# Optimization experiments

Measured on AMD Instinct MI355X. Metric: run time of the kernel, lower is better.

The kernel has to match this reference:

```python
import jax, jax.numpy as jnp
import numpy as np

DIM = 1024
N_HEADS = 16
HEAD_DIM = DIM // N_HEADS


def setup_inputs() -> dict:
    key = jax.random.key(0)
    ks = jax.random.split(key, 6)
    s = DIM ** -0.5
    return {
        "x": jax.random.normal(ks[0], (2, 2048, DIM), dtype=jnp.float32),
        "Wq": jax.random.normal(ks[1], (DIM, DIM), dtype=jnp.float32) * s,
        "Wk": jax.random.normal(ks[2], (DIM, DIM), dtype=jnp.float32) * s,
        "Wv": jax.random.normal(ks[3], (DIM, DIM), dtype=jnp.float32) * s,
        "Wo": jax.random.normal(ks[4], (DIM, DIM), dtype=jnp.float32) * s,
        "bo": jax.random.normal(ks[5], (DIM,), dtype=jnp.float32) * 0.01,
    }


def reference(x, Wq, Wk, Wv, Wo, bo):
    B, T, C = x.shape
    H, D = N_HEADS, HEAD_DIM
    # Linear(dim, dim, bias=False): y = x @ W^T
    q = (x @ Wq.T).reshape(B, T, H, D).transpose(0, 2, 1, 3)  # B H T D
    k = (x @ Wk.T).reshape(B, T, H, D).transpose(0, 2, 1, 3)
    v = (x @ Wv.T).reshape(B, T, H, D).transpose(0, 2, 1, 3)
    q = q * (D ** -0.5)
    attn = jnp.einsum('bhqd,bhkd->bhqk', q, k)  # B H T T
    causal_mask = jnp.triu(jnp.ones((T, T), dtype=bool), k=1)
    attn = jnp.where(causal_mask, -jnp.inf, attn)
    attn = jax.nn.softmax(attn, axis=-1)
    out = jnp.einsum('bhqk,bhkd->bhqd', attn, v)  # B H T D
    out = out.transpose(0, 2, 1, 3).reshape(B, T, C)
    return out @ Wo.T + bo
```

## Files before the change

kernel.cpp:

```cpp
#include <hip/hip_runtime.h>
#include <math.h>

typedef __attribute__((ext_vector_type(8))) short bf16x8;
typedef __attribute__((ext_vector_type(4))) float f32x4;
typedef __attribute__((ext_vector_type(16))) float f32x16;

__device__ __forceinline__ ushort f2bf(float f) {
  union { float f; unsigned u; } v; v.f = f;
  return (ushort)((v.u + 0x8000u) >> 16);
}

__device__ __forceinline__ void g2l16(const void* g, void* l) {
  __builtin_amdgcn_global_load_lds((const __attribute__((address_space(1))) unsigned*)g,
                                   (__attribute__((address_space(3))) unsigned*)l, 16, 0, 0);
}

__global__ __launch_bounds__(256) void cast_all(const float* __restrict__ x,
                                                const float* __restrict__ Wq,
                                                const float* __restrict__ Wk,
                                                const float* __restrict__ Wv,
                                                const float* __restrict__ Wo,
                                                ushort* __restrict__ xbf,
                                                ushort* __restrict__ wcat,
                                                float4* __restrict__ O32) {
  int i = blockIdx.x * 256 + threadIdx.x;
  if (i < 1048576) {
    float4 v = ((const float4*)x)[i];
    ushort4 u; u.x = f2bf(v.x); u.y = f2bf(v.y); u.z = f2bf(v.z); u.w = f2bf(v.w);
    ((ushort4*)xbf)[i] = u;
  } else if (i < 2097152) {
    int j = i - 1048576;
    int sel = j >> 18;
    const float* src = (sel == 0) ? Wq : (sel == 1) ? Wk : (sel == 2) ? Wv : Wo;
    float scale = (sel == 0) ? 0.125f * 1.44269504088896f : 1.0f;
    float4 v = ((const float4*)src)[j & 0x3FFFF];
    ushort4 u;
    u.x = f2bf(v.x * scale); u.y = f2bf(v.y * scale);
    u.z = f2bf(v.z * scale); u.w = f2bf(v.w * scale);
    ((ushort4*)wcat)[j] = u;
  } else {
    O32[i - 2097152] = float4{0.f, 0.f, 0.f, 0.f};
  }
}

__global__ __launch_bounds__(256) void gemm_qkv(const ushort* __restrict__ A,
                                                const ushort* __restrict__ B,
                                                ushort* __restrict__ C3,
                                                ushort* __restrict__ Vt) {
  const int K = 1024;
  __shared__ __align__(16) ushort smem[17408];
  ushort* As = smem;
  ushort* Bs = smem + 8192;
  const int m0 = blockIdx.y * 128, n0 = blockIdx.x * 128;
  const int tid = threadIdx.x, lane = tid & 63, wid = tid >> 6;
  const int quad = lane >> 4, lc = lane & 15;
  const int lrow = lane >> 2, lcol = (lane & 3) * 8;
  const int wm = (wid >> 1) * 64, wn = (wid & 1) * 64;

  f32x4 acc[4][4] = {};

  auto stage = [&](int k0, int nb) {
    const ushort* Ag = A + (size_t)(m0 + wid * 32 + lrow) * K + k0 + lcol;
    g2l16(Ag, &As[nb * 4096 + wid * 1024]);
    g2l16(Ag + (size_t)16 * K, &As[nb * 4096 + wid * 1024 + 512]);
    const ushort* Bg = B + (size_t)(n0 + wid * 32 + lrow) * K + k0 + lcol;
    g2l16(Bg, &Bs[nb * 4096 + wid * 1024]);
    g2l16(Bg + (size_t)16 * K, &Bs[nb * 4096 + wid * 1024 + 512]);
  };

  stage(0, 0);
  for (int k0 = 0; k0 < K; k0 += 32) {
    const int nb = (k0 >> 5) & 1;
    __syncthreads();
    if (k0 + 32 < K) stage(k0 + 32, nb ^ 1);

    bf16x8 af[4], bfr[4];
#pragma unroll
    for (int t = 0; t < 4; t++)
      af[t] = *(const bf16x8*)&As[nb * 4096 + (wm + t * 16 + lc) * 32 + quad * 8];
#pragma unroll
    for (int t = 0; t < 4; t++)
      bfr[t] = *(const bf16x8*)&Bs[nb * 4096 + (wn + t * 16 + lc) * 32 + quad * 8];
#pragma unroll
    for (int mt = 0; mt < 4; mt++)
#pragma unroll
      for (int nt = 0; nt < 4; nt++)
        acc[mt][nt] = __builtin_amdgcn_mfma_f32_16x16x32_bf16(af[mt], bfr[nt], acc[mt][nt], 0, 0, 0);
  }

  const int sel = n0 >> 10;
  if (sel < 2) {
#pragma unroll
    for (int mt = 0; mt < 4; mt++) {
#pragma unroll
      for (int r = 0; r < 4; r++) {
        int row = m0 + wm + mt * 16 + quad * 4 + r;
#pragma unroll
        for (int nt = 0; nt < 4; nt++) {
          int col = n0 + wn + nt * 16 + lc;
          size_t dst = ((size_t)sel << 22) + (size_t)row * 1024 + (col & 1023);
          C3[dst] = f2bf(acc[mt][nt][r]);
        }
      }
    }
  } else {
    __syncthreads();
#pragma unroll
    for (int mt = 0; mt < 4; mt++)
#pragma unroll
      for (int r = 0; r < 4; r++) {
        int tl = wm + mt * 16 + quad * 4 + r;
#pragma unroll
        for (int nt = 0; nt < 4; nt++)
          smem[(wn + nt * 16 + lc) * 136 + tl] = f2bf(acc[mt][nt][r]);
      }
    __syncthreads();
    const int hd0 = n0 - 2048, b = m0 >> 11, t_base = m0 & 2047;
#pragma unroll
    for (int i = 0; i < 8; i++) {
      int idx = i * 256 + tid;
      int dl = idx >> 4, tc = (idx & 15) * 8;
      uint4 v = *(const uint4*)&smem[dl * 136 + tc];
      int hd = hd0 + dl;
      *(uint4*)(Vt + (size_t)(b * 16 + (hd >> 6)) * 131072 +
                (size_t)(hd & 63) * 2048 + t_base + tc) = v;
    }
  }
}

__global__ __launch_bounds__(256) void gemm_proj(const ushort* __restrict__ A,
                                                 const ushort* __restrict__ B,
                                                 float* __restrict__ C,
                                                 const float* __restrict__ bias) {
  const int K = 1024;
  __shared__ __align__(16) ushort As[2][2][128 * 32];
  __shared__ __align__(16) ushort Bs[2][2][64 * 32];
  const int m0 = blockIdx.y * 128, n0 = blockIdx.x * 64;
  const int tid = threadIdx.x, lane = tid & 63, wid = tid >> 6;
  const int quad = lane >> 4, lc = lane & 15;
  const int lrow = lane >> 2, lcol = (lane & 3) * 8;
  const int wm = (wid >> 1) * 64, wn = (wid & 1) * 32;

  f32x4 acc[4][2] = {};

  auto stage = [&](int k0, int nb) {
    const ushort* Ag = A + (size_t)(m0 + wid * 32 + lrow) * K + k0 + lcol;
    g2l16(Ag,                       &As[nb][0][wid * 1024]);
    g2l16(Ag + (size_t)16 * K,      &As[nb][0][wid * 1024 + 512]);
    g2l16(Ag + 32,                  &As[nb][1][wid * 1024]);
    g2l16(Ag + (size_t)16 * K + 32, &As[nb][1][wid * 1024 + 512]);
    const ushort* Bg = B + (size_t)(n0 + wid * 16 + lrow) * K + k0 + lcol;
    g2l16(Bg,      &Bs[nb][0][wid * 512]);
    g2l16(Bg + 32, &Bs[nb][1][wid * 512]);
  };

  stage(0, 0);
  for (int k0 = 0; k0 < K; k0 += 64) {
    const int nb = (k0 >> 6) & 1;
    __syncthreads();
    if (k0 + 64 < K) stage(k0 + 64, nb ^ 1);

#pragma unroll
    for (int ks = 0; ks < 2; ks++) {
      bf16x8 af[4], bfr[2];
#pragma unroll
      for (int t = 0; t < 4; t++)
        af[t] = *(const bf16x8*)&As[nb][ks][(wm + t * 16 + lc) * 32 + quad * 8];
#pragma unroll
      for (int t = 0; t < 2; t++)
        bfr[t] = *(const bf16x8*)&Bs[nb][ks][(wn + t * 16 + lc) * 32 + quad * 8];
#pragma unroll
      for (int mt = 0; mt < 4; mt++)
#pragma unroll
        for (int nt = 0; nt < 2; nt++)
          acc[mt][nt] = __builtin_amdgcn_mfma_f32_16x16x32_bf16(af[mt], bfr[nt], acc[mt][nt], 0, 0, 0);
    }
  }

#pragma unroll
  for (int mt = 0; mt < 4; mt++) {
#pragma unroll
    for (int r = 0; r < 4; r++) {
      int row = m0 + wm + mt * 16 + quad * 4 + r;
#pragma unroll
      for (int nt = 0; nt < 2; nt++) {
        int col = n0 + wn + nt * 16 + lc;
        C[(size_t)row * 1024 + col] = acc[mt][nt][r] + bias[col];
      }
    }
  }
}

__global__ __launch_bounds__(256, 4) void attn_kernel(const ushort* __restrict__ Qb,
                                                      const ushort* __restrict__ Kb,
                                                      const ushort* __restrict__ Vt,
                                                      float* __restrict__ O32,
                                                      float* __restrict__ L32) {
  __shared__ __align__(16) ushort Ks[2][4096];
  __shared__ __align__(16) ushort Vs[2][4096];

  const int bh = blockIdx.y, b = bh >> 4, h = bh & 15;
  const int f = (int)blockIdx.x;
  int qi, ci;
  if (f < 16)      { qi = 12 + (f >> 2); ci = f & 3; }
  else if (f < 28) { int g = f - 16; int q3 = g / 3; qi = 8 + q3; ci = g - 3 * q3; }
  else if (f < 36) { int g = f - 28; qi = 4 + (g >> 1); ci = g & 1; }
  else             { qi = f - 36; ci = 0; }
  const int t0 = ci * 8;
  const int t1 = min(t0 + 8, 2 * qi + 2);

  const int tid = threadIdx.x, lane = tid & 63, wid = tid >> 6;
  const int hi = lane >> 5, ln = lane & 31;
  const int qbw = qi * 128 + wid * 32;
  const int qg = qbw + ln;

  const size_t kbase = (size_t)(b * 2048) * 1024 + h * 64;
  const size_t vbase = (size_t)bh * 131072;

  bf16x8 qf[4];
  {
    const ushort* Qp = Qb + kbase + (size_t)qg * 1024 + hi * 8;
#pragma unroll
    for (int dc = 0; dc < 4; dc++)
      qf[dc] = *(const bf16x8*)(Qp + dc * 16);
  }

  f32x16 o_acc[2] = {};
  float l_own = 0.f;

  const int krow = lane >> 3, kcol = lane & 7;
  const int dsw = (kcol ^ krow) << 3;

  auto stage = [&](int kb, int nb) {
    const ushort* gK = Kb + kbase + (size_t)(kb + wid * 8 + krow) * 1024 + dsw;
    g2l16(gK, &Ks[nb][wid * 512]);
    g2l16(gK + (size_t)32 * 1024, &Ks[nb][2048 + wid * 512]);
    const ushort* gV = Vt + vbase + (size_t)(wid * 8 + krow) * 2048 + kb + dsw;
    g2l16(gV, &Vs[nb][wid * 512]);
    g2l16(gV + (size_t)32 * 2048, &Vs[nb][2048 + wid * 512]);
  };

  const int sx = ln & 7;

  stage(t0 * 64, 0);
  for (int kt = t0; kt < t1; kt++) {
    const int kb = kt * 64;
    const int nb = (kt - t0) & 1;
    __syncthreads();
    if (kt + 1 < t1) stage(kb + 64, nb ^ 1);
    if (kb > qbw + 31) continue;

    const ushort* ks = &Ks[nb][0];
    const ushort* vs = &Vs[nb][0];

    unsigned pa[4][4];
#pragma unroll
    for (int g64 = 0; g64 < 2; g64++) {
      f32x16 s;
#pragma unroll
      for (int z = 0; z < 16; z++) s[z] = 0.f;
#pragma unroll
      for (int dc = 0; dc < 4; dc++) {
        bf16x8 kf = *(const bf16x8*)&ks[(g64 * 32 + ln) * 64 + (((dc * 2 + hi) ^ sx) << 3)];
        s = __builtin_amdgcn_mfma_f32_32x32x16_bf16(kf, qf[dc], s, 0, 0, 0);
      }
      const bool dmask = (kb + g64 * 32 + 31 > qbw);
      unsigned U[8];
#pragma unroll
      for (int g = 0; g < 4; g++) {
        float e[4];
#pragma unroll
        for (int j = 0; j < 4; j++) {
          float sv = s[g * 4 + j];
          if (dmask && (kb + g64 * 32 + g * 8 + hi * 4 + j > qg)) sv = -1e30f;
          e[j] = __builtin_amdgcn_exp2f(sv);
        }
        ushort b0 = f2bf(e[0]), b1 = f2bf(e[1]), b2 = f2bf(e[2]), b3 = f2bf(e[3]);
        U[g * 2]     = (unsigned)b0 | ((unsigned)b1 << 16);
        U[g * 2 + 1] = (unsigned)b2 | ((unsigned)b3 << 16);
      }
#pragma unroll
      for (int t = 0; t < 8; t++) {
        union { unsigned u; float f; } plo, phi;
        plo.u = U[t] << 16;
        phi.u = U[t] & 0xffff0000u;
        l_own += plo.f + phi.f;
      }
#pragma unroll
      for (int half = 0; half < 2; half++)
#pragma unroll
        for (int w = 0; w < 4; w++)
          pa[g64 * 2 + half][w] = U[half * 4 + w];
    }

#pragma unroll
    for (int m = 0; m < 4; m++) {
      bf16x8 pfrag;
#pragma unroll
      for (int w = 0; w < 4; w++) ((unsigned*)&pfrag)[w] = pa[m][w];
#pragma unroll
      for (int dg = 0; dg < 2; dg++) {
        const ushort* vrow = &vs[(dg * 32 + ln) * 64];
        bf16x8 vbf;
        *(unsigned long long*)&vbf =
            *(const unsigned long long*)&vrow[(((2 * m) ^ sx) << 3) + 4 * hi];
        *((unsigned long long*)&vbf + 1) =
            *(const unsigned long long*)&vrow[(((2 * m + 1) ^ sx) << 3) + 4 * hi];
        o_acc[dg] = __builtin_amdgcn_mfma_f32_32x32x16_bf16(pfrag, vbf, o_acc[dg], 0, 0, 0);
      }
    }
  }

  {
    float lt = l_own + __shfl_xor(l_own, 32);
    if (hi == 0) atomicAdd(&L32[(size_t)bh * 2048 + qg], lt);
  }
#pragma unroll
  for (int r = 0; r < 16; r++) {
    int q = qbw + (r & 3) + ((r >> 2) << 3) + hi * 4;
    size_t orow = ((size_t)(b * 2048) + q) * 1024 + h * 64 + ln;
    atomicAdd(&O32[orow], o_acc[0][r]);
    atomicAdd(&O32[orow + 32], o_acc[1][r]);
  }
}

__global__ __launch_bounds__(256) void normalize_kernel(const float* __restrict__ O32,
                                                        const float* __restrict__ L32,
                                                        ushort* __restrict__ Out) {
  const int row = blockIdx.x;
  const int tid = threadIdx.x;
  const int col = tid * 4;
  const int b = row >> 11, t = row & 2047, h = col >> 6;
  const float inv = 1.0f / L32[(size_t)(b * 16 + h) * 2048 + t];
  float4 o = ((const float4*)(O32 + (size_t)row * 1024))[tid];
  ushort4 u;
  u.x = f2bf(o.x * inv); u.y = f2bf(o.y * inv);
  u.z = f2bf(o.z * inv); u.w = f2bf(o.w * inv);
  ((ushort4*)(Out + (size_t)row * 1024))[tid] = u;
}

extern "C" void kernel_launch(void* const* d_in, const int* in_sizes, int n_in,
                              void* d_out, int out_size, void* d_ws, size_t ws_size,
                              hipStream_t stream) {
  const float* x  = (const float*)d_in[0];
  const float* Wq = (const float*)d_in[1];
  const float* Wk = (const float*)d_in[2];
  const float* Wv = (const float*)d_in[3];
  const float* Wo = (const float*)d_in[4];
  const float* bo = (const float*)d_in[5];
  float* out = (float*)d_out;

  char* ws = (char*)d_ws;
  ushort* xbf  = (ushort*)(ws);
  ushort* wcat = (ushort*)(ws + (8ull  << 20));
  ushort* qkv  = (ushort*)(ws + (16ull << 20));
  ushort* Qp   = qkv;
  ushort* Kp   = qkv + (1ull << 22);
  ushort* Vt   = qkv + (2ull << 22);
  float*  L32  = (float*)ws;
  float*  O32  = out;
  ushort* attn_out = Qp;

  cast_all<<<12288, 256, 0, stream>>>(x, Wq, Wk, Wv, Wo, xbf, wcat, (float4*)O32);

  gemm_qkv<<<dim3(24, 32), 256, 0, stream>>>(xbf, wcat, qkv, Vt);

  hipMemsetAsync(L32, 0, (size_t)32 * 2048 * 4, stream);

  attn_kernel<<<dim3(40, 32), 256, 0, stream>>>(Qp, Kp, Vt, O32, L32);

  normalize_kernel<<<4096, 256, 0, stream>>>(O32, L32, attn_out);

  gemm_proj<<<dim3(16, 32), 256, 0, stream>>>(
      attn_out, wcat + (size_t)3072 * 1024, out, bo);
}
```

Baseline: 200.8 us.

## Triple-buffer attention K/V staging with explicit vmcnt waits and MFMA priority

The attention kernel moves from double to triple buffered K/V tiles in LDS, prefetching two tiles ahead and waiting with explicit s_waitcnt vmcnt instead of a plain __syncthreads. MFMA sections are wrapped in s_setprio to favour matrix issue. The grid is transposed so consecutive blocks cover different heads at the same chunk index. The row-sum now accumulates fp32 exp values instead of the bf16-rounded ones. The extra LDS lowers occupancy to 3 blocks per CU, and the hand-written wait counts depend on the exact number of loads issued per stage.

```diff
diff --git a/kernel.cpp b/kernel.cpp
--- a/kernel.cpp
+++ b/kernel.cpp
@@ -191,16 +191,16 @@
   }
 }
 
-__global__ __launch_bounds__(256, 4) void attn_kernel(const ushort* __restrict__ Qb,
+__global__ __launch_bounds__(256, 3) void attn_kernel(const ushort* __restrict__ Qb,
                                                       const ushort* __restrict__ Kb,
                                                       const ushort* __restrict__ Vt,
                                                       float* __restrict__ O32,
                                                       float* __restrict__ L32) {
-  __shared__ __align__(16) ushort Ks[2][4096];
-  __shared__ __align__(16) ushort Vs[2][4096];
-
-  const int bh = blockIdx.y, b = bh >> 4, h = bh & 15;
-  const int f = (int)blockIdx.x;
+  __shared__ __align__(16) ushort Ks[3][4096];
+  __shared__ __align__(16) ushort Vs[3][4096];
+
+  const int bh = blockIdx.x, b = bh >> 4, h = bh & 15;
+  const int f = (int)blockIdx.y;
   int qi, ci;
   if (f < 16)      { qi = 12 + (f >> 2); ci = f & 3; }
   else if (f < 28) { int g = f - 16; int q3 = g / 3; qi = 8 + q3; ci = g - 3 * q3; }
@@ -224,6 +224,7 @@
     for (int dc = 0; dc < 4; dc++)
       qf[dc] = *(const bf16x8*)(Qp + dc * 16);
   }
+  asm volatile("" :: "v"(qf[0]), "v"(qf[1]), "v"(qf[2]), "v"(qf[3]));
 
   f32x16 o_acc[2] = {};
   float l_own = 0.f;
@@ -243,72 +244,79 @@
   const int sx = ln & 7;
 
   stage(t0 * 64, 0);
+  if (t0 + 1 < t1) stage(t0 * 64 + 64, 1);
+  int nb = 0;
   for (int kt = t0; kt < t1; kt++) {
     const int kb = kt * 64;
-    const int nb = (kt - t0) & 1;
-    __syncthreads();
-    if (kt + 1 < t1) stage(kb + 64, nb ^ 1);
-    if (kb > qbw + 31) continue;
-
-    const ushort* ks = &Ks[nb][0];
-    const ushort* vs = &Vs[nb][0];
-
-    unsigned pa[4][4];
-#pragma unroll
-    for (int g64 = 0; g64 < 2; g64++) {
-      f32x16 s;
-#pragma unroll
-      for (int z = 0; z < 16; z++) s[z] = 0.f;
-#pragma unroll
-      for (int dc = 0; dc < 4; dc++) {
-        bf16x8 kf = *(const bf16x8*)&ks[(g64 * 32 + ln) * 64 + (((dc * 2 + hi) ^ sx) << 3)];
-        s = __builtin_amdgcn_mfma_f32_32x32x16_bf16(kf, qf[dc], s, 0, 0, 0);
-      }
-      const bool dmask = (kb + g64 * 32 + 31 > qbw);
-      unsigned U[8];
-#pragma unroll
-      for (int g = 0; g < 4; g++) {
-        float e[4];
-#pragma unroll
-        for (int j = 0; j < 4; j++) {
-          float sv = s[g * 4 + j];
-          if (dmask && (kb + g64 * 32 + g * 8 + hi * 4 + j > qg)) sv = -1e30f;
-          e[j] = __builtin_amdgcn_exp2f(sv);
+    if (kt + 1 < t1) asm volatile("s_waitcnt vmcnt(4)" ::: "memory");
+    else             asm volatile("s_waitcnt vmcnt(0)" ::: "memory");
+    __builtin_amdgcn_s_barrier();
+    __builtin_amdgcn_sched_barrier(0);
+    if (kt + 2 < t1) {
+      int sb = (nb >= 1) ? nb - 1 : 2;
+      stage(kb + 128, sb);
+    }
+
+    if (kb <= qbw + 31) {
+      const ushort* ks = &Ks[nb][0];
+      const ushort* vs = &Vs[nb][0];
+
+      unsigned pa[4][4];
+#pragma unroll
+      for (int g64 = 0; g64 < 2; g64++) {
+        f32x16 s;
+#pragma unroll
+        for (int z = 0; z < 16; z++) s[z] = 0.f;
+        __builtin_amdgcn_s_setprio(1);
+#pragma unroll
+        for (int dc = 0; dc < 4; dc++) {
+          bf16x8 kf = *(const bf16x8*)&ks[(g64 * 32 + ln) * 64 + (((dc * 2 + hi) ^ sx) << 3)];
+          s = __builtin_amdgcn_mfma_f32_32x32x16_bf16(kf, qf[dc], s, 0, 0, 0);
         }
-        ushort b0 = f2bf(e[0]), b1 = f2bf(e[1]), b2 = f2bf(e[2]), b3 = f2bf(e[3]);
-        U[g * 2]     = (unsigned)b0 | ((unsigned)b1 << 16);
-        U[g * 2 + 1] = (unsigned)b2 | ((unsigned)b3 << 16);
-      }
-#pragma unroll
-      for (int t = 0; t < 8; t++) {
-        union { unsigned u; float f; } plo, phi;
-        plo.u = U[t] << 16;
-        phi.u = U[t] & 0xffff0000u;
-        l_own += plo.f + phi.f;
-      }
-#pragma unroll
-      for (int half = 0; half < 2; half++)
-#pragma unroll
-        for (int w = 0; w < 4; w++)
-          pa[g64 * 2 + half][w] = U[half * 4 + w];
-    }
-
-#pragma unroll
-    for (int m = 0; m < 4; m++) {
-      bf16x8 pfrag;
-#pragma unroll
-      for (int w = 0; w < 4; w++) ((unsigned*)&pfrag)[w] = pa[m][w];
-#pragma unroll
-      for (int dg = 0; dg < 2; dg++) {
-        const ushort* vrow = &vs[(dg * 32 + ln) * 64];
-        bf16x8 vbf;
-        *(unsigned long long*)&vbf =
-            *(const unsigned long long*)&vrow[(((2 * m) ^ sx) << 3) + 4 * hi];
-        *((unsigned long long*)&vbf + 1) =
-            *(const unsigned long long*)&vrow[(((2 * m + 1) ^ sx) << 3) + 4 * hi];
-        o_acc[dg] = __builtin_amdgcn_mfma_f32_32x32x16_bf16(pfrag, vbf, o_acc[dg], 0, 0, 0);
-      }
-    }
+        __builtin_amdgcn_s_setprio(0);
+        const bool dmask = (kb + g64 * 32 + 31 > qbw);
+        unsigned U[8];
+#pragma unroll
+        for (int g = 0; g < 4; g++) {
+          float e[4];
+#pragma unroll
+          for (int j = 0; j < 4; j++) {
+            float sv = s[g * 4 + j];
+            if (dmask && (kb + g64 * 32 + g * 8 + hi * 4 + j > qg)) sv = -1e30f;
+            e[j] = __builtin_amdgcn_exp2f(sv);
+          }
+          l_own += (e[0] + e[1]) + (e[2] + e[3]);
+          ushort b0 = f2bf(e[0]), b1 = f2bf(e[1]), b2 = f2bf(e[2]), b3 = f2bf(e[3]);
+          U[g * 2]     = (unsigned)b0 | ((unsigned)b1 << 16);
+          U[g * 2 + 1] = (unsigned)b2 | ((unsigned)b3 << 16);
+        }
+#pragma unroll
+        for (int half = 0; half < 2; half++)
+#pragma unroll
+          for (int w = 0; w < 4; w++)
+            pa[g64 * 2 + half][w] = U[half * 4 + w];
+      }
+
+      __builtin_amdgcn_s_setprio(1);
+#pragma unroll
+      for (int m = 0; m < 4; m++) {
+        bf16x8 pfrag;
+#pragma unroll
+        for (int w = 0; w < 4; w++) ((unsigned*)&pfrag)[w] = pa[m][w];
+#pragma unroll
+        for (int dg = 0; dg < 2; dg++) {
+          const ushort* vrow = &vs[(dg * 32 + ln) * 64];
+          bf16x8 vbf;
+          *(unsigned long long*)&vbf =
+              *(const unsigned long long*)&vrow[(((2 * m) ^ sx) << 3) + 4 * hi];
+          *((unsigned long long*)&vbf + 1) =
+              *(const unsigned long long*)&vrow[(((2 * m + 1) ^ sx) << 3) + 4 * hi];
+          o_acc[dg] = __builtin_amdgcn_mfma_f32_32x32x16_bf16(pfrag, vbf, o_acc[dg], 0, 0, 0);
+        }
+      }
+      __builtin_amdgcn_s_setprio(0);
+    }
+    nb = (nb == 2) ? 0 : nb + 1;
   }
 
   {
@@ -367,7 +375,7 @@
 
   hipMemsetAsync(L32, 0, (size_t)32 * 2048 * 4, stream);
 
-  attn_kernel<<<dim3(40, 32), 256, 0, stream>>>(Qp, Kp, Vt, O32, L32);
+  attn_kernel<<<dim3(32, 40), 256, 0, stream>>>(Qp, Kp, Vt, O32, L32);
 
   normalize_kernel<<<4096, 256, 0, stream>>>(O32, L32, attn_out);
 
```

Result: no change. 199.5 us (-0.6%).
